# Kernel optimization log

Measured on AMD Instinct MI355X. Metric: run time of the kernel, lower is better.

Reference implementation:

```python
import jax, jax.numpy as jnp
import numpy as np

B, S, D, H, FF, P = 16, 200, 512, 8, 2048, 10
HD = D // H
EPS = 1e-5


def _pe2d(h, w, ch):
    # Faithful numpy port of PositionalEncoding2D (positional_encodings lib)
    channels = int(np.ceil(ch / 4) * 2)
    inv_freq = 1.0 / (10000.0 ** (np.arange(0, channels, 2, dtype=np.float32) / channels))
    sin_x = np.einsum('i,j->ij', np.arange(h, dtype=np.float32), inv_freq)
    sin_y = np.einsum('i,j->ij', np.arange(w, dtype=np.float32), inv_freq)
    emb_x = np.stack([np.sin(sin_x), np.cos(sin_x)], -1).reshape(h, channels)
    emb_y = np.stack([np.sin(sin_y), np.cos(sin_y)], -1).reshape(w, channels)
    emb = np.zeros((h, w, 2 * channels), dtype=np.float32)
    emb[:, :, :channels] = emb_x[:, None, :]
    emb[:, :, channels:2 * channels] = emb_y[None, :, :]
    return emb[:, :, :ch]


def _xavier(key, shape):
    fan_out, fan_in = shape
    lim = float(np.sqrt(6.0 / (fan_in + fan_out)))
    return jax.random.uniform(key, shape, minval=-lim, maxval=lim, dtype=jnp.float32)


def setup_inputs():
    key = jax.random.key(0)
    ks = jax.random.split(key, 8)
    x = jax.random.normal(ks[0], (B, S, D), dtype=jnp.float32)
    pos = jnp.asarray(_pe2d(S, S, P))  # (S, S, P) positional bias features
    Wkv = _xavier(ks[1], (2 * D, D)); bkv = jnp.zeros((2 * D,))
    Wo = _xavier(ks[2], (D, D)); bo = jnp.zeros((D,))
    Wpos = _xavier(ks[3], (1, P)); bpos = jnp.zeros((1,))
    W1 = _xavier(ks[4], (FF, D)); b1 = jnp.zeros((FF,))
    W2 = _xavier(ks[5], (D, FF)); b2 = jnp.zeros((D,))
    g1 = jnp.ones((D,)); beta1 = jnp.zeros((D,))
    g2 = jnp.ones((D,)); beta2 = jnp.zeros((D,))
    return {"x": x, "pos": pos, "Wkv": Wkv, "bkv": bkv, "Wo": Wo, "bo": bo,
            "Wpos": Wpos, "bpos": bpos, "W1": W1, "b1": b1, "W2": W2, "b2": b2,
            "g1": g1, "beta1": beta1, "g2": g2, "beta2": beta2}


def _layernorm(x, g, b):
    mu = jnp.mean(x, axis=-1, keepdims=True)
    var = jnp.mean(jnp.square(x - mu), axis=-1, keepdims=True)
    return (x - mu) * jax.lax.rsqrt(var + EPS) * g + b


def reference(x, pos, Wkv, bkv, Wo, bo, Wpos, bpos, W1, b1, W2, b2, g1, beta1, g2, beta2):
    # --- MultiheadAttention_KV (attn_type='kv') ---
    kv = x @ Wkv.T + bkv                                   # (B,S,2D)
    kv = kv.reshape(B, S, H, 2 * HD).transpose(0, 2, 1, 3)  # (B,H,S,2hd)
    k, v = kv[..., :HD], kv[..., HD:]
    attn = jnp.einsum('bhid,bhjd->bhij', k, k) / jnp.sqrt(jnp.float32(HD))
    # map_pos is linear: map_pos(attn[...,None] + pos) == attn*sum(w) + (pos@w + b)
    # -> same math as materializing the (B,H,S,S,P) tensor, but fused.
    pos_bias = pos @ Wpos[0] + bpos[0]                     # (S,S)
    scores = attn * jnp.sum(Wpos) + pos_bias[None, None]
    a = jax.nn.softmax(scores, axis=-1)
    vals = jnp.einsum('bhij,bhjd->bhid', a, v)             # (B,H,S,hd)
    vals = vals.transpose(0, 2, 1, 3).reshape(B, S, D)
    o = vals @ Wo.T + bo
    # --- residual + post-norm ---
    h = _layernorm(x + o, g1, beta1)
    # --- FFN ---
    ff = jax.nn.relu(h @ W1.T + b1) @ W2.T + b2
    return _layernorm(h + ff, g2, beta2)
```

## Files before the change

kernel.cpp:

```cpp
#include <hip/hip_runtime.h>
#include <hip/hip_bf16.h>

#define EPSV 1e-5f
static const int B_ = 16, S_ = 200, D_ = 512, H_ = 8, FF_ = 2048, P_ = 10, HD_ = 64;
static const int SP = 224;

typedef __bf16 bf16_t;
typedef __attribute__((ext_vector_type(8))) __bf16 bf16x8;
typedef __attribute__((ext_vector_type(4))) __bf16 bf16x4;
typedef __attribute__((ext_vector_type(4))) float f32x4;

__device__ __forceinline__ void gload16(const void* g, void* l) {
    __builtin_amdgcn_global_load_lds(
        (const __attribute__((address_space(1))) void*)g,
        (__attribute__((address_space(3))) void*)l, 16, 0, 0);
}

template <int BM, int BN, int WROWS, int WCOLS, int EPI>
__global__ __launch_bounds__(256) void mfma_gemm(
    const bf16_t* __restrict__ A,
    const bf16_t* __restrict__ Bw,
    float* __restrict__ Cf, bf16_t* __restrict__ Cb, long cBat, int ldc,
    const float* __restrict__ bias,
    bf16_t* __restrict__ kOut, bf16_t* __restrict__ vtOut,
    int M, int N, int K, int kcPerSplit)
{
    constexpr int MR = WROWS / 16, NR = WCOLS / 16;
    constexpr int NWC = BN / WCOLS;
    constexpr int NLOADS = BM / 32 + BN / 32;
    static_assert((4 / NWC) * WROWS == BM, "wave tiling must cover BM");
    static_assert(NWC * WCOLS == BN, "wave tiling must cover BN");
    static_assert(NLOADS == 6, "vmcnt literal below assumes 6 loads/stage");

    __shared__ bf16_t Asm[2][BM * 64];
    __shared__ bf16_t Bsm[2][BN * 64];

    const int wv = threadIdx.x >> 6;
    const int ln = threadIdx.x & 63;
    const int split = blockIdx.z;
    const int rowBase = blockIdx.y * BM;
    const int colBase = blockIdx.x * BN;
    const int wr = (wv / NWC) * WROWS;
    const int wc = (wv % NWC) * WCOLS;

    const int lr8 = ln >> 3;
    const int csw = ((ln & 7) ^ lr8) * 8;

    f32x4 acc[MR][NR] = {};

    const int kBeg = split * kcPerSplit;
    const int kEnd = kBeg + kcPerSplit;

    auto STAGE = [&](int k0, int buf) {
        #pragma unroll
        for (int i = 0; i < BM / 32; i++) {
            int row = i * 32 + wv * 8 + lr8;
            int gr = rowBase + row; gr = (gr < M) ? gr : (M - 1);
            gload16(A + (long)gr * K + k0 + csw, &Asm[buf][(i * 32 + wv * 8) * 64]);
        }
        #pragma unroll
        for (int i = 0; i < BN / 32; i++) {
            int col = i * 32 + wv * 8 + lr8;
            int gc = colBase + col; gc = (gc < N) ? gc : (N - 1);
            gload16(Bw + (long)gc * K + k0 + csw, &Bsm[buf][(i * 32 + wv * 8) * 64]);
        }
    };

    auto COMPUTE = [&](int buf) {
        #pragma unroll
        for (int kk = 0; kk < 2; kk++) {
            bf16x8 af[MR], bfr[NR];
            #pragma unroll
            for (int m = 0; m < MR; m++) {
                int r = wr + m * 16 + (ln & 15);
                int pc = (kk * 4 + (ln >> 4)) ^ (r & 7);
                af[m] = *reinterpret_cast<const bf16x8*>(&Asm[buf][r * 64 + pc * 8]);
            }
            #pragma unroll
            for (int n = 0; n < NR; n++) {
                int r = wc + n * 16 + (ln & 15);
                int pc = (kk * 4 + (ln >> 4)) ^ (r & 7);
                bfr[n] = *reinterpret_cast<const bf16x8*>(&Bsm[buf][r * 64 + pc * 8]);
            }
            #pragma unroll
            for (int m = 0; m < MR; m++)
                #pragma unroll
                for (int n = 0; n < NR; n++)
                    acc[m][n] = __builtin_amdgcn_mfma_f32_16x16x32_bf16(
                        af[m], bfr[n], acc[m][n], 0, 0, 0);
        }
    };

    STAGE(kBeg, 0);

    int t = 0;
    for (int k0 = kBeg; k0 < kEnd; k0 += 64, ++t) {
        const bool has_next = (k0 + 64 < kEnd);
        if (has_next) {
            STAGE(k0 + 64, (t + 1) & 1);
            asm volatile("s_waitcnt vmcnt(6)" ::: "memory");
        } else {
            asm volatile("s_waitcnt vmcnt(0)" ::: "memory");
        }
        __builtin_amdgcn_s_barrier();
        __builtin_amdgcn_sched_barrier(0);
        COMPUTE(t & 1);
        if (has_next) {
            __builtin_amdgcn_sched_barrier(0);
            __builtin_amdgcn_s_barrier();
        }
    }

    #pragma unroll
    for (int m = 0; m < MR; m++) {
        #pragma unroll
        for (int n = 0; n < NR; n++) {
            #pragma unroll
            for (int r = 0; r < 4; r++) {
                int row = rowBase + wr + m * 16 + (ln >> 4) * 4 + r;
                int col = colBase + wc + n * 16 + (ln & 15);
                if (row >= M || col >= N) continue;
                float v = acc[m][n][r];
                if constexpr (EPI == 3) {
                    v += bias[col];
                    int b = row / S_, s = row - b * S_;
                    int h = col >> 7, w = col & 127;
                    if (w < HD_)
                        kOut[((long)(b * H_ + h) * SP + s) * HD_ + w] = (bf16_t)v;
                    else
                        vtOut[((long)(b * H_ + h) * HD_ + (w - HD_)) * SP + s] = (bf16_t)v;
                } else if constexpr (EPI == 1) {
                    v += bias[col];
                    v = fmaxf(v, 0.f);
                    Cb[(long)row * ldc + col] = (bf16_t)v;
                } else {
                    Cf[(long)split * cBat + (long)row * ldc + col] = v;
                }
            }
        }
    }
}

__global__ __launch_bounds__(256) void attn_fused(
    const bf16_t* __restrict__ Kb, const bf16_t* __restrict__ Vt,
    const float* __restrict__ G, const float* __restrict__ scalePtr,
    bf16_t* __restrict__ vals)
{
    __shared__ __align__(16) bf16_t Pl[4][16][232];

    const int bh = blockIdx.x;
    const int tile = blockIdx.y;
    const int wv = threadIdx.x >> 6;
    const int ln = threadIdx.x & 63;
    const int b = bh >> 3, h = bh & 7;
    const int rowBase = tile * 64 + wv * 16;

    const bf16_t* Kbh = Kb + (long)bh * SP * HD_;
    const bf16_t* Vbh = Vt + (long)bh * HD_ * SP;
    const float scale = scalePtr[0];

    const int lr = ln & 15;
    const int lk = (ln >> 4) * 8;

    f32x4 acc[14];
    #pragma unroll
    for (int n = 0; n < 14; n++) acc[n] = (f32x4){0.f, 0.f, 0.f, 0.f};

    int arow = rowBase + lr; arow = (arow < S_) ? arow : (S_ - 1);
    const bf16x8 a0 = *reinterpret_cast<const bf16x8*>(Kbh + (long)arow * HD_ + lk);
    const bf16x8 a1 = *reinterpret_cast<const bf16x8*>(Kbh + (long)arow * HD_ + 32 + lk);

    #pragma unroll
    for (int n = 0; n < 14; n++) {
        const bf16_t* bp = Kbh + (long)(n * 16 + lr) * HD_;
        bf16x8 b0 = *reinterpret_cast<const bf16x8*>(bp + lk);
        bf16x8 b1 = *reinterpret_cast<const bf16x8*>(bp + 32 + lk);
        acc[n] = __builtin_amdgcn_mfma_f32_16x16x32_bf16(a0, b0, acc[n], 0, 0, 0);
        acc[n] = __builtin_amdgcn_mfma_f32_16x16x32_bf16(a1, b1, acc[n], 0, 0, 0);
    }

    float Gc[14];
    #pragma unroll
    for (int n = 0; n < 14; n++) Gc[n] = G[n * 16 + lr];

    #pragma unroll
    for (int r = 0; r < 4; r++) {
        float m = -1e30f;
        #pragma unroll
        for (int n = 0; n < 14; n++) {
            float v = acc[n][r] * scale + Gc[n];
            acc[n][r] = v;
            m = fmaxf(m, v);
        }
        #pragma unroll
        for (int off = 1; off < 16; off <<= 1) m = fmaxf(m, __shfl_xor(m, off));
        float s = 0.f;
        #pragma unroll
        for (int n = 0; n < 14; n++) {
            float e = __expf(acc[n][r] - m);
            acc[n][r] = e;
            s += e;
        }
        #pragma unroll
        for (int off = 1; off < 16; off <<= 1) s += __shfl_xor(s, off);
        float inv = 1.f / s;
        #pragma unroll
        for (int n = 0; n < 14; n++) acc[n][r] *= inv;
    }

    #pragma unroll
    for (int n = 0; n < 14; n++)
        #pragma unroll
        for (int r = 0; r < 4; r++)
            Pl[wv][(ln >> 4) * 4 + r][n * 16 + lr] = (bf16_t)acc[n][r];

    f32x4 vacc[4] = {};
    #pragma unroll
    for (int kk = 0; kk < 7; kk++) {
        bf16x8 pa = *reinterpret_cast<const bf16x8*>(&Pl[wv][lr][kk * 32 + lk]);
        #pragma unroll
        for (int n = 0; n < 4; n++) {
            bf16x8 vb = *reinterpret_cast<const bf16x8*>(
                Vbh + (long)(n * 16 + lr) * SP + kk * 32 + lk);
            vacc[n] = __builtin_amdgcn_mfma_f32_16x16x32_bf16(pa, vb, vacc[n], 0, 0, 0);
        }
    }

    #pragma unroll
    for (int n = 0; n < 4; n++) {
        #pragma unroll
        for (int r = 0; r < 4; r++) {
            int row = rowBase + (ln >> 4) * 4 + r;
            if (row < S_)
                vals[((long)b * S_ + row) * D_ + h * HD_ + n * 16 + lr] =
                    (bf16_t)vacc[n][r];
        }
    }
}

__global__ __launch_bounds__(256) void prep_all(
    const float* __restrict__ x, const float* __restrict__ Wkv,
    const float* __restrict__ Wo, const float* __restrict__ W1,
    const float* __restrict__ W2, bf16_t* __restrict__ dst,
    float4* __restrict__ zeroP,
    const float* __restrict__ pos, const float* __restrict__ Wpos,
    float* __restrict__ G, float* __restrict__ scal)
{
    const int gid = blockIdx.x * blockDim.x + threadIdx.x;
    const int nthr = gridDim.x * blockDim.x;

    for (int i = gid; i < 1130496; i += nthr) {
        long e = (long)i * 4;
        const float* s; long off;
        if (e < 1638400)      { s = x;   off = e; }
        else if (e < 2162688) { s = Wkv; off = e - 1638400; }
        else if (e < 2424832) { s = Wo;  off = e - 2162688; }
        else if (e < 3473408) { s = W1;  off = e - 2424832; }
        else                  { s = W2;  off = e - 3473408; }
        float4 v = *reinterpret_cast<const float4*>(s + off);
        bf16x4 o = {(bf16_t)v.x, (bf16_t)v.y, (bf16_t)v.z, (bf16_t)v.w};
        *reinterpret_cast<bf16x4*>(dst + e) = o;
    }
    for (int i = gid; i < 458752; i += nthr)
        zeroP[i] = make_float4(0.f, 0.f, 0.f, 0.f);
    if (gid < SP) {
        float g = -1e30f;
        if (gid < S_) {
            g = 0.f;
            #pragma unroll
            for (int p = 6; p < 10; p++) g += pos[(long)gid * P_ + p] * Wpos[p];
        }
        G[gid] = g;
    }
    if (gid == 0) {
        float sw = 0.f;
        for (int p = 0; p < P_; p++) sw += Wpos[p];
        scal[0] = sw * 0.125f;
    }
}

template <int NPART>
__global__ __launch_bounds__(256) void add_ln_p(
    const float* __restrict__ a, const float* __restrict__ parts, long partStride,
    const float* __restrict__ bias,
    const float* __restrict__ g, const float* __restrict__ beta,
    float* __restrict__ outf, bf16_t* __restrict__ outb, int rows)
{
    int row = blockIdx.x * 4 + (threadIdx.x >> 6);
    int lane = threadIdx.x & 63;
    if (row >= rows) return;
    long base = (long)row * D_;
    float v[8];
    float sum = 0.f;
    #pragma unroll
    for (int i = 0; i < 8; i++) {
        int c = lane + i * 64;
        float t = a[base + c] + bias[c];
        #pragma unroll
        for (int p = 0; p < NPART; p++) t += parts[p * partStride + base + c];
        v[i] = t;
        sum += t;
    }
    #pragma unroll
    for (int off = 32; off; off >>= 1) sum += __shfl_xor(sum, off);
    float mean = sum * (1.f / 512.f);
    float var = 0.f;
    #pragma unroll
    for (int i = 0; i < 8; i++) { float d = v[i] - mean; var += d * d; }
    #pragma unroll
    for (int off = 32; off; off >>= 1) var += __shfl_xor(var, off);
    float rstd = rsqrtf(var * (1.f / 512.f) + EPSV);
    #pragma unroll
    for (int i = 0; i < 8; i++) {
        int c = lane + i * 64;
        float o = (v[i] - mean) * rstd * g[c] + beta[c];
        outf[base + c] = o;
        if (outb) outb[base + c] = (bf16_t)o;
    }
}

extern "C" void kernel_launch(void* const* d_in, const int* in_sizes, int n_in,
                              void* d_out, int out_size, void* d_ws, size_t ws_size,
                              hipStream_t stream)
{
    const float* x    = (const float*)d_in[0];
    const float* pos  = (const float*)d_in[1];
    const float* Wkv  = (const float*)d_in[2];
    const float* bkv  = (const float*)d_in[3];
    const float* Wo   = (const float*)d_in[4];
    const float* bo   = (const float*)d_in[5];
    const float* Wpos = (const float*)d_in[6];
    const float* W1   = (const float*)d_in[8];
    const float* b1   = (const float*)d_in[9];
    const float* W2   = (const float*)d_in[10];
    const float* b2   = (const float*)d_in[11];
    const float* g1   = (const float*)d_in[12];
    const float* be1  = (const float*)d_in[13];
    const float* g2   = (const float*)d_in[14];
    const float* be2  = (const float*)d_in[15];
    float* out = (float*)d_out;

    char* w = (char*)d_ws;
    bf16_t* xb   = (bf16_t*)(w + 0);
    bf16_t* Wkvb = (bf16_t*)(w + 3276800);
    bf16_t* Wob  = (bf16_t*)(w + 4325376);
    bf16_t* W1b  = (bf16_t*)(w + 4849664);
    bf16_t* W2b  = (bf16_t*)(w + 6946816);
    bf16_t* Kb   = (bf16_t*)(w + 9043968);
    bf16_t* Vt   = (bf16_t*)(w + 12713984);
    float*  G    = (float*)(w + 16384000);
    float*  scal = (float*)(w + 16384896);
    bf16_t* vals = (bf16_t*)(w + 16385024);
    float*  hf   = (float*)(w + 19661824);
    bf16_t* hb   = (bf16_t*)(w + 26215424);
    float*  obuf = (float*)(w + 29492224);
    bf16_t* tb   = (bf16_t*)(w + 42599424);
    float*  fbuf = (float*)(w + 55706624);

    const int M = B_ * S_;
    const long PS = (long)M * D_;

    prep_all<<<2048, 256, 0, stream>>>(x, Wkv, Wo, W1, W2, xb, (float4*)Kb,
                                       pos, Wpos, G, scal);

    mfma_gemm<128, 64, 64, 32, 3><<<dim3(16, 25, 1), 256, 0, stream>>>(
        xb, Wkvb, nullptr, nullptr, 0, 0, bkv, Kb, Vt, M, 2 * D_, D_, D_);

    attn_fused<<<dim3(128, 4, 1), 256, 0, stream>>>(Kb, Vt, G, scal, vals);

    mfma_gemm<128, 64, 64, 32, 5><<<dim3(8, 25, 2), 256, 0, stream>>>(
        vals, Wob, obuf, nullptr, PS, D_, nullptr, nullptr, nullptr, M, D_, D_, 256);

    add_ln_p<2><<<(M + 3) / 4, 256, 0, stream>>>(x, obuf, PS, bo, g1, be1, hf, hb, M);

    mfma_gemm<128, 64, 64, 32, 1><<<dim3(32, 25, 1), 256, 0, stream>>>(
        hb, W1b, nullptr, tb, 0, FF_, b1, nullptr, nullptr, M, FF_, D_, D_);

    mfma_gemm<128, 64, 64, 32, 5><<<dim3(8, 25, 2), 256, 0, stream>>>(
        tb, W2b, fbuf, nullptr, PS, D_, nullptr, nullptr, nullptr, M, D_, FF_, 1024);

    add_ln_p<2><<<(M + 3) / 4, 256, 0, stream>>>(hf, fbuf, PS, b2, g2, be2, out, nullptr, M);
}
```

Before: 116.6 us.

## Store split-K partials and residuals in bf16, vectorize layernorm loads/stores

The split-K GEMM partial outputs for the Wo and W2 projections are now written as bf16 instead of fp32. Both add+layernorm kernels read bf16 inputs, including the bf16 copy of x and the bf16 h as residuals, using 16-byte vector loads and stores. The fp32 copy of h is dropped, so the second layernorm uses the bf16 residual. This roughly halves memory traffic between the GEMMs and the layernorms, at the cost of extra rounding on the partial sums and residuals.

```diff
diff --git a/kernel.cpp b/kernel.cpp
--- a/kernel.cpp
+++ b/kernel.cpp
@@ -20,7 +20,7 @@
 __global__ __launch_bounds__(256) void mfma_gemm(
     const bf16_t* __restrict__ A,
     const bf16_t* __restrict__ Bw,
-    float* __restrict__ Cf, bf16_t* __restrict__ Cb, long cBat, int ldc,
+    bf16_t* __restrict__ Cb, long cBat, int ldc,
     const float* __restrict__ bias,
     bf16_t* __restrict__ kOut, bf16_t* __restrict__ vtOut,
     int M, int N, int K, int kcPerSplit)
@@ -134,7 +134,7 @@
                     v = fmaxf(v, 0.f);
                     Cb[(long)row * ldc + col] = (bf16_t)v;
                 } else {
-                    Cf[(long)split * cBat + (long)row * ldc + col] = v;
+                    Cb[(long)split * cBat + (long)row * ldc + col] = (bf16_t)v;
                 }
             }
         }
@@ -279,9 +279,9 @@
     }
 }
 
-template <int NPART>
-__global__ __launch_bounds__(256) void add_ln_p(
-    const float* __restrict__ a, const float* __restrict__ parts, long partStride,
+template <int NPART, bool F32OUT>
+__global__ __launch_bounds__(256) void add_ln_v(
+    const bf16_t* __restrict__ a, const bf16_t* __restrict__ parts, long partStride,
     const float* __restrict__ bias,
     const float* __restrict__ g, const float* __restrict__ beta,
     float* __restrict__ outf, bf16_t* __restrict__ outb, int rows)
@@ -289,15 +289,26 @@
     int row = blockIdx.x * 4 + (threadIdx.x >> 6);
     int lane = threadIdx.x & 63;
     if (row >= rows) return;
-    long base = (long)row * D_;
+    const int col = lane * 8;
+    const long base = (long)row * D_ + col;
+
+    bf16x8 a8 = *reinterpret_cast<const bf16x8*>(a + base);
+    float4 b0 = *reinterpret_cast<const float4*>(bias + col);
+    float4 b1 = *reinterpret_cast<const float4*>(bias + col + 4);
+    const float bb[8] = {b0.x, b0.y, b0.z, b0.w, b1.x, b1.y, b1.z, b1.w};
+
+    bf16x8 p8[NPART];
+    #pragma unroll
+    for (int p = 0; p < NPART; p++)
+        p8[p] = *reinterpret_cast<const bf16x8*>(parts + (long)p * partStride + base);
+
     float v[8];
     float sum = 0.f;
     #pragma unroll
     for (int i = 0; i < 8; i++) {
-        int c = lane + i * 64;
-        float t = a[base + c] + bias[c];
-        #pragma unroll
-        for (int p = 0; p < NPART; p++) t += parts[p * partStride + base + c];
+        float t = (float)a8[i] + bb[i];
+        #pragma unroll
+        for (int p = 0; p < NPART; p++) t += (float)p8[p][i];
         v[i] = t;
         sum += t;
     }
@@ -310,12 +321,28 @@
     #pragma unroll
     for (int off = 32; off; off >>= 1) var += __shfl_xor(var, off);
     float rstd = rsqrtf(var * (1.f / 512.f) + EPSV);
-    #pragma unroll
-    for (int i = 0; i < 8; i++) {
-        int c = lane + i * 64;
-        float o = (v[i] - mean) * rstd * g[c] + beta[c];
-        outf[base + c] = o;
-        if (outb) outb[base + c] = (bf16_t)o;
+
+    float4 g0 = *reinterpret_cast<const float4*>(g + col);
+    float4 g1v = *reinterpret_cast<const float4*>(g + col + 4);
+    float4 e0 = *reinterpret_cast<const float4*>(beta + col);
+    float4 e1 = *reinterpret_cast<const float4*>(beta + col + 4);
+    const float gg[8] = {g0.x, g0.y, g0.z, g0.w, g1v.x, g1v.y, g1v.z, g1v.w};
+    const float ee[8] = {e0.x, e0.y, e0.z, e0.w, e1.x, e1.y, e1.z, e1.w};
+
+    if constexpr (F32OUT) {
+        float4 o0, o1;
+        o0.x = (v[0]-mean)*rstd*gg[0]+ee[0]; o0.y = (v[1]-mean)*rstd*gg[1]+ee[1];
+        o0.z = (v[2]-mean)*rstd*gg[2]+ee[2]; o0.w = (v[3]-mean)*rstd*gg[3]+ee[3];
+        o1.x = (v[4]-mean)*rstd*gg[4]+ee[4]; o1.y = (v[5]-mean)*rstd*gg[5]+ee[5];
+        o1.z = (v[6]-mean)*rstd*gg[6]+ee[6]; o1.w = (v[7]-mean)*rstd*gg[7]+ee[7];
+        *reinterpret_cast<float4*>(outf + base) = o0;
+        *reinterpret_cast<float4*>(outf + base + 4) = o1;
+    } else {
+        bf16x8 o8;
+        #pragma unroll
+        for (int i = 0; i < 8; i++)
+            o8[i] = (bf16_t)((v[i] - mean) * rstd * gg[i] + ee[i]);
+        *reinterpret_cast<bf16x8*>(outb + base) = o8;
     }
 }
 
@@ -341,21 +368,20 @@
     float* out = (float*)d_out;
 
     char* w = (char*)d_ws;
-    bf16_t* xb   = (bf16_t*)(w + 0);
-    bf16_t* Wkvb = (bf16_t*)(w + 3276800);
-    bf16_t* Wob  = (bf16_t*)(w + 4325376);
-    bf16_t* W1b  = (bf16_t*)(w + 4849664);
-    bf16_t* W2b  = (bf16_t*)(w + 6946816);
-    bf16_t* Kb   = (bf16_t*)(w + 9043968);
-    bf16_t* Vt   = (bf16_t*)(w + 12713984);
-    float*  G    = (float*)(w + 16384000);
-    float*  scal = (float*)(w + 16384896);
-    bf16_t* vals = (bf16_t*)(w + 16385024);
-    float*  hf   = (float*)(w + 19661824);
-    bf16_t* hb   = (bf16_t*)(w + 26215424);
-    float*  obuf = (float*)(w + 29492224);
-    bf16_t* tb   = (bf16_t*)(w + 42599424);
-    float*  fbuf = (float*)(w + 55706624);
+    bf16_t* xb     = (bf16_t*)(w + 0);
+    bf16_t* Wkvb   = (bf16_t*)(w + 3276800);
+    bf16_t* Wob    = (bf16_t*)(w + 4325376);
+    bf16_t* W1b    = (bf16_t*)(w + 4849664);
+    bf16_t* W2b    = (bf16_t*)(w + 6946816);
+    bf16_t* Kb     = (bf16_t*)(w + 9043968);
+    bf16_t* Vt     = (bf16_t*)(w + 12713984);
+    float*  G      = (float*)(w + 16384000);
+    float*  scal   = (float*)(w + 16384896);
+    bf16_t* vals   = (bf16_t*)(w + 16385024);
+    bf16_t* hb     = (bf16_t*)(w + 19661824);
+    bf16_t* obuf_b = (bf16_t*)(w + 22938624);
+    bf16_t* tb     = (bf16_t*)(w + 29492224);
+    bf16_t* fbuf_b = (bf16_t*)(w + 42599424);
 
     const int M = B_ * S_;
     const long PS = (long)M * D_;
@@ -364,20 +390,22 @@
                                        pos, Wpos, G, scal);
 
     mfma_gemm<128, 64, 64, 32, 3><<<dim3(16, 25, 1), 256, 0, stream>>>(
-        xb, Wkvb, nullptr, nullptr, 0, 0, bkv, Kb, Vt, M, 2 * D_, D_, D_);
+        xb, Wkvb, nullptr, 0, 0, bkv, Kb, Vt, M, 2 * D_, D_, D_);
 
     attn_fused<<<dim3(128, 4, 1), 256, 0, stream>>>(Kb, Vt, G, scal, vals);
 
     mfma_gemm<128, 64, 64, 32, 5><<<dim3(8, 25, 2), 256, 0, stream>>>(
-        vals, Wob, obuf, nullptr, PS, D_, nullptr, nullptr, nullptr, M, D_, D_, 256);
-
-    add_ln_p<2><<<(M + 3) / 4, 256, 0, stream>>>(x, obuf, PS, bo, g1, be1, hf, hb, M);
+        vals, Wob, obuf_b, PS, D_, nullptr, nullptr, nullptr, M, D_, D_, 256);
+
+    add_ln_v<2, false><<<(M + 3) / 4, 256, 0, stream>>>(
+        xb, obuf_b, PS, bo, g1, be1, nullptr, hb, M);
 
     mfma_gemm<128, 64, 64, 32, 1><<<dim3(32, 25, 1), 256, 0, stream>>>(
-        hb, W1b, nullptr, tb, 0, FF_, b1, nullptr, nullptr, M, FF_, D_, D_);
+        hb, W1b, tb, 0, FF_, b1, nullptr, nullptr, M, FF_, D_, D_);
 
     mfma_gemm<128, 64, 64, 32, 5><<<dim3(8, 25, 2), 256, 0, stream>>>(
-        tb, W2b, fbuf, nullptr, PS, D_, nullptr, nullptr, nullptr, M, D_, FF_, 1024);
-
-    add_ln_p<2><<<(M + 3) / 4, 256, 0, stream>>>(hf, fbuf, PS, b2, g2, be2, out, nullptr, M);
-}
+        tb, W2b, fbuf_b, PS, D_, nullptr, nullptr, nullptr, M, D_, FF_, 1024);
+
+    add_ln_v<2, true><<<(M + 3) / 4, 256, 0, stream>>>(
+        hb, fbuf_b, PS, b2, g2, be2, out, nullptr, M);
+}
```

Measured after the change: 109.3 us. -6.3%, faster.
